# Performance work log

Hardware: AMD Instinct MI355X
Metric: run time of the kernel (lower is better)

The kernel has to match this reference:

```python
import jax, jax.numpy as jnp
import numpy as np

B, C, CI, T, H, W = 2, 1024, 512, 32, 14, 14
N = T * H * W


def setup_inputs() -> dict:
    key = jax.random.key(0)
    ks = jax.random.split(key, 6)
    s_in = 1.0 / np.sqrt(C)
    s_mid = 1.0 / np.sqrt(CI)
    return {
        "x": jax.random.normal(ks[0], (B, C, T, H, W), jnp.float32),
        "Wk": jax.random.normal(ks[1], (CI, C), jnp.float32) * s_in,
        "bk": jnp.zeros((CI,), jnp.float32),
        "Wq": jax.random.normal(ks[2], (CI, C), jnp.float32) * s_in,
        "bq": jnp.zeros((CI,), jnp.float32),
        "Wv": jax.random.normal(ks[3], (CI, C), jnp.float32) * s_in,
        "bv": jnp.zeros((CI,), jnp.float32),
        "Wo": jax.random.normal(ks[4], (C, CI), jnp.float32) * s_mid,
        "bo": jnp.zeros((C,), jnp.float32),
    }


def reference(x, Wk, bk, Wq, bq, Wv, bv, Wo, bo):
    # x: (B, C, T, H, W). Dropout layers are identity at inference.
    b, c, t, h, w = x.shape
    n = t * h * w
    xf = x.reshape(b, c, n)                          # (B, C, N)
    k = jnp.einsum("dc,bcn->bdn", Wk, xf) + bk[None, :, None]   # (B, CI, N)
    q = jnp.einsum("dc,bcn->bdn", Wq, xf) + bq[None, :, None]   # (B, CI, N)
    v = jnp.einsum("dc,bcn->bdn", Wv, xf) + bv[None, :, None]   # (B, CI, N)
    # alpha[b,i,j] = sum_d key[b,i,d] * query[b,d,j], scaled by 1/T
    alpha = jnp.einsum("bdi,bdj->bij", k, q) / float(t)          # (B, N, N)
    alpha = jax.nn.softmax(alpha, axis=-1)
    # y (B, CI, N) with y[b,c,i] = sum_j alpha[b,i,j] * v[b,c,j]
    y = jnp.einsum("bij,bcj->bci", alpha, v)
    out = jnp.einsum("dc,bcn->bdn", Wo, y) + bo[None, :, None]   # (B, C, N)
    return out.reshape(b, c, t, h, w) + x
```

## Files before the change

### kernel.cpp

```cpp
#include <hip/hip_runtime.h>

#define Bb 2
#define Cc 1024
#define CIi 512
#define Nn 6272
#define JH 3136
#define SCALE (1.0f / 32.0f)

typedef __bf16 bf16;
typedef __bf16 bf16x8 __attribute__((ext_vector_type(8)));
typedef __bf16 bf16x4 __attribute__((ext_vector_type(4)));
typedef float f32x4 __attribute__((ext_vector_type(4)));
typedef float f32x2 __attribute__((ext_vector_type(2)));
typedef unsigned int u32;
typedef unsigned int u32x4 __attribute__((ext_vector_type(4)));

__device__ __forceinline__ void g2l16(const void* g, void* l) {
  __builtin_amdgcn_global_load_lds(
      (const __attribute__((address_space(1))) u32*)g,
      (__attribute__((address_space(3))) u32*)(size_t)l, 16, 0, 0);
}

__global__ __launch_bounds__(256) void xpose_kernel(const float* __restrict__ x,
                                                    bf16* __restrict__ xT) {
  __shared__ float tile[32][33];
  int b = blockIdx.z;
  int n0 = blockIdx.x * 32, c0 = blockIdx.y * 32;
  int tn = threadIdx.x & 31, tr = threadIdx.x >> 5;
  const float* xp = x + ((size_t)b * Cc + c0) * Nn + n0;
  for (int i = 0; i < 4; i++) {
    int c = tr + i * 8;
    tile[c][tn] = xp[(size_t)c * Nn + tn];
  }
  __syncthreads();
  bf16* op = xT + ((size_t)b * Nn + n0) * Cc + c0;
  for (int i = 0; i < 4; i++) {
    int n = tr + i * 8;
    op[(size_t)n * Cc + tn] = (bf16)tile[tn][n];
  }
}

__global__ __launch_bounds__(256) void proj_kernel(
    const bf16* __restrict__ xT, const float* __restrict__ Wk,
    const float* __restrict__ Wq, const float* __restrict__ Wv,
    const float* __restrict__ bk, const float* __restrict__ bq,
    const float* __restrict__ bv, bf16* __restrict__ kT, bf16* __restrict__ qT,
    bf16* __restrict__ vv) {
  int z = blockIdx.z;
  int b = z / 3, proj = z % 3;
  const float* W = proj == 0 ? Wk : (proj == 1 ? Wq : Wv);
  const float* bias = proj == 0 ? bk : (proj == 1 ? bq : bv);
  int m0 = blockIdx.x * 128;
  int d0 = blockIdx.y * 128;
  __shared__ __align__(16) bf16 la[128 * 40];
  __shared__ __align__(16) bf16 lb[128 * 40];
  int tid = threadIdx.x;
  int wave = tid >> 6, lane = tid & 63, quad = lane >> 4, l16 = lane & 15;
  int wm = (wave >> 1) * 64, wn = (wave & 1) * 64;
  int row2 = tid >> 1, half = tid & 1;

  f32x4 acc[4][4] = {};
  const bf16* aSrc = xT + ((size_t)b * Nn + m0) * Cc;
  const float* bSrc = W + (size_t)(d0 + row2) * Cc;

  for (int k0 = 0; k0 < Cc; k0 += 32) {
    const u32x4* ga = (const u32x4*)(aSrc + (size_t)row2 * Cc + k0 + half * 16);
    u32x4 a0 = ga[0], a1 = ga[1];
    const f32x4* gb = (const f32x4*)(bSrc + k0 + half * 16);
    f32x4 w0 = gb[0], w1 = gb[1], w2 = gb[2], w3 = gb[3];
    *(u32x4*)&la[row2 * 40 + half * 16] = a0;
    *(u32x4*)&la[row2 * 40 + half * 16 + 8] = a1;
    bf16x8 p0 = {(bf16)w0[0], (bf16)w0[1], (bf16)w0[2], (bf16)w0[3],
                 (bf16)w1[0], (bf16)w1[1], (bf16)w1[2], (bf16)w1[3]};
    bf16x8 p1 = {(bf16)w2[0], (bf16)w2[1], (bf16)w2[2], (bf16)w2[3],
                 (bf16)w3[0], (bf16)w3[1], (bf16)w3[2], (bf16)w3[3]};
    *(bf16x8*)&lb[row2 * 40 + half * 16] = p0;
    *(bf16x8*)&lb[row2 * 40 + half * 16 + 8] = p1;
    __syncthreads();
    bf16x8 af[4], bfr[4];
    for (int t = 0; t < 4; t++)
      af[t] = *(const bf16x8*)&la[(wm + t * 16 + l16) * 40 + quad * 8];
    for (int t = 0; t < 4; t++)
      bfr[t] = *(const bf16x8*)&lb[(wn + t * 16 + l16) * 40 + quad * 8];
    for (int tm = 0; tm < 4; tm++)
      for (int tn = 0; tn < 4; tn++)
        acc[tm][tn] = __builtin_amdgcn_mfma_f32_16x16x32_bf16(
            af[tm], bfr[tn], acc[tm][tn], 0, 0, 0);
    __syncthreads();
  }
  for (int tn = 0; tn < 4; tn++) {
    int dcol = d0 + wn + tn * 16 + l16;
    float bval = bias[dcol];
    for (int tm = 0; tm < 4; tm++) {
      int nbase = m0 + wm + tm * 16 + quad * 4;
      for (int r = 0; r < 4; r++) {
        float val = acc[tm][tn][r] + bval;
        int nrow = nbase + r;
        if (proj == 0) {
          kT[((size_t)b * Nn + nrow) * CIi + dcol] = (bf16)val;
        } else if (proj == 1) {
          int ch = (dcol >> 3) ^ (nrow & 7);
          qT[((size_t)b * Nn + nrow) * CIi + ch * 8 + (dcol & 7)] = (bf16)val;
        } else {
          vv[((size_t)b * CIi + dcol) * Nn + nrow] = (bf16)val;
        }
      }
    }
  }
}

__global__ __launch_bounds__(512, 2) void attn_kernel(
    const bf16* __restrict__ kT, const bf16* __restrict__ qTs,
    const bf16* __restrict__ vv, bf16* __restrict__ yp,
    float* __restrict__ ml) {
  int l = blockIdx.x;
  int jh = l & 1, b = (l >> 1) & 1;
  int i0 = (l >> 2) * 128;
  int tid = threadIdx.x;
  int wave = tid >> 6, lane = tid & 63, quad = lane >> 4, l16 = lane & 15;
  int dw = wave * 64;

  __shared__ __align__(16) bf16 lq[2][32 * 512];
  __shared__ __align__(16) bf16 Psm[128 * 36];
  __shared__ float red[128];

  const bf16* qb = qTs + ((size_t)b * Nn + (size_t)jh * JH) * CIi;
  const bf16* vb = vv + (size_t)b * CIi * Nn + (size_t)jh * JH;

  bf16x8 kf[16];
  {
    const bf16* kp =
        kT + ((size_t)b * Nn + i0 + wave * 16 + l16) * CIi + quad * 8;
#pragma unroll
    for (int kk = 0; kk < 16; kk++) kf[kk] = *(const bf16x8*)(kp + kk * 32);
  }
  f32x4 oacc[8][4] = {};
  f32x4 l_acc = {};

  {
    const bf16* qrow = qb + (size_t)(wave * 4) * CIi + lane * 8;
#pragma unroll
    for (int r = 0; r < 4; r++)
      g2l16(qrow + (size_t)r * CIi, &lq[0][(wave * 4 + r) * 512]);
  }
  __syncthreads();

  int x0 = l16 & 7;
  for (int j0 = 0; j0 < JH; j0 += 32) {
    int t = (j0 >> 5) & 1;
    if (j0 + 32 < JH) {
      const bf16* qrow = qb + (size_t)(j0 + 32 + wave * 4) * CIi + lane * 8;
#pragma unroll
      for (int r = 0; r < 4; r++)
        g2l16(qrow + (size_t)r * CIi, &lq[t ^ 1][(wave * 4 + r) * 512]);
    }
    f32x4 s0 = {}, s1 = {};
    {
      const bf16* q0 = &lq[t][l16 * 512];
      const bf16* q1 = &lq[t][(16 + l16) * 512];
#pragma unroll
      for (int kk = 0; kk < 16; kk++) {
        int ch = (((kk * 4 + quad) ^ x0)) * 8;
        bf16x8 qf0 = *(const bf16x8*)(q0 + ch);
        bf16x8 qf1 = *(const bf16x8*)(q1 + ch);
        s0 = __builtin_amdgcn_mfma_f32_16x16x32_bf16(kf[kk], qf0, s0, 0, 0, 0);
        s1 = __builtin_amdgcn_mfma_f32_16x16x32_bf16(kf[kk], qf1, s1, 0, 0, 0);
      }
    }
    {
#pragma unroll
      for (int r = 0; r < 4; r++) {
        float p0 = __expf(fminf(fmaf(s0[r], SCALE, -2.0f), 20.0f));
        float p1 = __expf(fminf(fmaf(s1[r], SCALE, -2.0f), 20.0f));
        l_acc[r] += p0 + p1;
        int gi = wave * 16 + quad * 4 + r;
        Psm[gi * 36 + l16] = (bf16)p0;
        Psm[gi * 36 + 16 + l16] = (bf16)p1;
      }
    }
    __syncthreads();

    {
      u32x4 vf[4];
#pragma unroll
      for (int ds = 0; ds < 4; ds++)
        vf[ds] = *(const u32x4*)(vb + (size_t)(dw + ds * 16 + l16) * Nn + j0 +
                                 quad * 8);
#pragma unroll
      for (int is = 0; is < 8; is++) {
        bf16x8 pf = *(const bf16x8*)&Psm[(is * 16 + l16) * 36 + quad * 8];
#pragma unroll
        for (int ds = 0; ds < 4; ds++)
          oacc[is][ds] = __builtin_amdgcn_mfma_f32_16x16x32_bf16(
              pf, __builtin_bit_cast(bf16x8, vf[ds]), oacc[is][ds], 0, 0, 0);
      }
    }
    __syncthreads();
  }

#pragma unroll
  for (int o = 1; o < 16; o <<= 1)
#pragma unroll
    for (int r = 0; r < 4; r++) l_acc[r] += __shfl_xor(l_acc[r], o);
  if (l16 == 0) {
#pragma unroll
    for (int r = 0; r < 4; r++) {
      int gi = wave * 16 + quad * 4 + r;
      ml[(size_t)(jh * Bb + b) * Nn + i0 + gi] = l_acc[r];
      red[gi] = 1.0f / l_acc[r];
    }
  }
  __syncthreads();
  bf16* ypb = yp + ((size_t)jh * Bb + b) * Nn * CIi;
#pragma unroll
  for (int is = 0; is < 8; is++) {
    f32x4 inv = *(const f32x4*)&red[is * 16 + quad * 4];
#pragma unroll
    for (int ds = 0; ds < 4; ds++)
#pragma unroll
      for (int r = 0; r < 4; r++)
        ypb[(size_t)(i0 + is * 16 + quad * 4 + r) * CIi + dw + ds * 16 + l16] =
            (bf16)(oacc[is][ds][r] * inv[r]);
  }
}

__global__ __launch_bounds__(256) void merge_kernel(const bf16* __restrict__ yp,
                                                    const float* __restrict__ ml,
                                                    bf16* __restrict__ y) {
  int idx = blockIdx.x * 256 + threadIdx.x;
  int row = idx >> 6, c = idx & 63;
  float l0 = ml[row];
  float l1 = ml[(size_t)Bb * Nn + row];
  float inv = 1.0f / (l0 + l1);
  float w0 = l0 * inv, w1 = l1 * inv;
  bf16x8 v0 = *(const bf16x8*)&yp[(size_t)row * CIi + c * 8];
  bf16x8 v1 =
      *(const bf16x8*)&yp[(size_t)Bb * Nn * CIi + (size_t)row * CIi + c * 8];
  bf16x8 o;
#pragma unroll
  for (int k = 0; k < 8; k++)
    o[k] = (bf16)(w0 * (float)v0[k] + w1 * (float)v1[k]);
  *(bf16x8*)&y[(size_t)row * CIi + c * 8] = o;
}

__global__ __launch_bounds__(256) void out_kernel(
    const bf16* __restrict__ y, const float* __restrict__ Wo,
    const float* __restrict__ bo, const float* __restrict__ x,
    float* __restrict__ out) {
  int b = blockIdx.z;
  int d0 = blockIdx.x * 128;
  int m0 = blockIdx.y * 128;
  __shared__ __align__(16) bf16 la[128 * 40];
  __shared__ __align__(16) bf16 lb[128 * 40];
  int tid = threadIdx.x;
  int wave = tid >> 6, lane = tid & 63, quad = lane >> 4, l16 = lane & 15;
  int wm = (wave >> 1) * 64, wn = (wave & 1) * 64;
  int row2 = tid >> 1, half = tid & 1;
  f32x4 acc[4][4] = {};
  const float* aSrc = Wo + (size_t)(d0 + row2) * CIi;
  const bf16* bSrc = y + ((size_t)b * Nn + m0 + row2) * CIi;
  for (int k0 = 0; k0 < CIi; k0 += 32) {
    const f32x4* ga = (const f32x4*)(aSrc + k0 + half * 16);
    f32x4 w0 = ga[0], w1 = ga[1], w2 = ga[2], w3 = ga[3];
    const u32x4* gb = (const u32x4*)(bSrc + k0 + half * 16);
    u32x4 b0 = gb[0], b1 = gb[1];
    bf16x8 p0 = {(bf16)w0[0], (bf16)w0[1], (bf16)w0[2], (bf16)w0[3],
                 (bf16)w1[0], (bf16)w1[1], (bf16)w1[2], (bf16)w1[3]};
    bf16x8 p1 = {(bf16)w2[0], (bf16)w2[1], (bf16)w2[2], (bf16)w2[3],
                 (bf16)w3[0], (bf16)w3[1], (bf16)w3[2], (bf16)w3[3]};
    *(bf16x8*)&la[row2 * 40 + half * 16] = p0;
    *(bf16x8*)&la[row2 * 40 + half * 16 + 8] = p1;
    *(u32x4*)&lb[row2 * 40 + half * 16] = b0;
    *(u32x4*)&lb[row2 * 40 + half * 16 + 8] = b1;
    __syncthreads();
    bf16x8 af[4], bfr[4];
    for (int t = 0; t < 4; t++)
      af[t] = *(const bf16x8*)&la[(wm + t * 16 + l16) * 40 + quad * 8];
    for (int t = 0; t < 4; t++)
      bfr[t] = *(const bf16x8*)&lb[(wn + t * 16 + l16) * 40 + quad * 8];
    for (int tm = 0; tm < 4; tm++)
      for (int tn = 0; tn < 4; tn++)
        acc[tm][tn] = __builtin_amdgcn_mfma_f32_16x16x32_bf16(
            af[tm], bfr[tn], acc[tm][tn], 0, 0, 0);
    __syncthreads();
  }
  for (int tm = 0; tm < 4; tm++) {
    for (int r = 0; r < 4; r++) {
      int drow = d0 + wm + tm * 16 + quad * 4 + r;
      float bval = bo[drow];
      const float* xrow = x + ((size_t)b * Cc + drow) * Nn;
      float* orow = out + ((size_t)b * Cc + drow) * Nn;
      for (int tn = 0; tn < 4; tn++) {
        int ncol = m0 + wn + tn * 16 + l16;
        orow[ncol] = acc[tm][tn][r] + bval + xrow[ncol];
      }
    }
  }
}

extern "C" void kernel_launch(void* const* d_in, const int* in_sizes, int n_in,
                              void* d_out, int out_size, void* d_ws,
                              size_t ws_size, hipStream_t stream) {
  (void)in_sizes;
  (void)n_in;
  (void)out_size;
  (void)ws_size;
  const float* x = (const float*)d_in[0];
  const float* Wk = (const float*)d_in[1];
  const float* bk = (const float*)d_in[2];
  const float* Wq = (const float*)d_in[3];
  const float* bq = (const float*)d_in[4];
  const float* Wv = (const float*)d_in[5];
  const float* bv = (const float*)d_in[6];
  const float* Wo = (const float*)d_in[7];
  const float* bo = (const float*)d_in[8];
  float* out = (float*)d_out;

  bf16* xT = (bf16*)d_ws;
  bf16* yp = (bf16*)d_ws;
  bf16* y = (bf16*)d_ws + (size_t)Bb * Nn * Cc;
  bf16* kT = (bf16*)d_out;
  bf16* qT = kT + (size_t)Bb * Nn * CIi;
  bf16* vv = qT + (size_t)Bb * Nn * CIi;
  float* ml = (float*)((char*)d_out + (size_t)40 * 1024 * 1024);

  xpose_kernel<<<dim3(Nn / 32, Cc / 32, Bb), 256, 0, stream>>>(x, xT);
  proj_kernel<<<dim3(Nn / 128, CIi / 128, 3 * Bb), 256, 0, stream>>>(
      xT, Wk, Wq, Wv, bk, bq, bv, kT, qT, vv);
  attn_kernel<<<dim3((Nn / 128) * 2 * Bb), 512, 0, stream>>>(kT, qT, vv, yp,
                                                             ml);
  merge_kernel<<<dim3(Bb * Nn * 64 / 256), 256, 0, stream>>>(yp, ml, y);
  out_kernel<<<dim3(Cc / 128, Nn / 128, Bb), 256, 0, stream>>>(y, Wo, bo, x,
                                                               out);
}
```

Baseline: 579.3 us.

## Split attention key range into four partitions instead of two

The attention kernel now splits the key/value range into four quarters instead of two, doubling the grid so more workgroups are available to fill the CUs. The merge kernel combines four partial outputs, weighted by their softmax denominators. The occupancy hint rises from 2 to 4 blocks, which squeezes the per-thread register budget while each thread still holds large accumulator and K-fragment arrays, so spilling is a real risk. LDS use per block limits actual residency anyway, and the larger partial buffer means the merged output now aliases part of the partial-result workspace.

```diff
diff --git a/kernel.cpp b/kernel.cpp
--- a/kernel.cpp
+++ b/kernel.cpp
@@ -4,7 +4,7 @@
 #define Cc 1024
 #define CIi 512
 #define Nn 6272
-#define JH 3136
+#define JQ 1568
 #define SCALE (1.0f / 32.0f)
 
 typedef __bf16 bf16;
@@ -109,13 +109,13 @@
   }
 }
 
-__global__ __launch_bounds__(512, 2) void attn_kernel(
+__global__ __launch_bounds__(512, 4) void attn_kernel(
     const bf16* __restrict__ kT, const bf16* __restrict__ qTs,
     const bf16* __restrict__ vv, bf16* __restrict__ yp,
     float* __restrict__ ml) {
   int l = blockIdx.x;
-  int jh = l & 1, b = (l >> 1) & 1;
-  int i0 = (l >> 2) * 128;
+  int jq = l & 3, b = (l >> 2) & 1;
+  int i0 = (l >> 3) * 128;
   int tid = threadIdx.x;
   int wave = tid >> 6, lane = tid & 63, quad = lane >> 4, l16 = lane & 15;
   int dw = wave * 64;
@@ -124,8 +124,8 @@
   __shared__ __align__(16) bf16 Psm[128 * 36];
   __shared__ float red[128];
 
-  const bf16* qb = qTs + ((size_t)b * Nn + (size_t)jh * JH) * CIi;
-  const bf16* vb = vv + (size_t)b * CIi * Nn + (size_t)jh * JH;
+  const bf16* qb = qTs + ((size_t)b * Nn + (size_t)jq * JQ) * CIi;
+  const bf16* vb = vv + (size_t)b * CIi * Nn + (size_t)jq * JQ;
 
   bf16x8 kf[16];
   {
@@ -146,9 +146,9 @@
   __syncthreads();
 
   int x0 = l16 & 7;
-  for (int j0 = 0; j0 < JH; j0 += 32) {
+  for (int j0 = 0; j0 < JQ; j0 += 32) {
     int t = (j0 >> 5) & 1;
-    if (j0 + 32 < JH) {
+    if (j0 + 32 < JQ) {
       const bf16* qrow = qb + (size_t)(j0 + 32 + wave * 4) * CIi + lane * 8;
 #pragma unroll
       for (int r = 0; r < 4; r++)
@@ -206,12 +206,12 @@
 #pragma unroll
     for (int r = 0; r < 4; r++) {
       int gi = wave * 16 + quad * 4 + r;
-      ml[(size_t)(jh * Bb + b) * Nn + i0 + gi] = l_acc[r];
+      ml[(size_t)(jq * Bb + b) * Nn + i0 + gi] = l_acc[r];
       red[gi] = 1.0f / l_acc[r];
     }
   }
   __syncthreads();
-  bf16* ypb = yp + ((size_t)jh * Bb + b) * Nn * CIi;
+  bf16* ypb = yp + ((size_t)jq * Bb + b) * Nn * CIi;
 #pragma unroll
   for (int is = 0; is < 8; is++) {
     f32x4 inv = *(const f32x4*)&red[is * 16 + quad * 4];
@@ -229,17 +229,27 @@
                                                     bf16* __restrict__ y) {
   int idx = blockIdx.x * 256 + threadIdx.x;
   int row = idx >> 6, c = idx & 63;
-  float l0 = ml[row];
-  float l1 = ml[(size_t)Bb * Nn + row];
-  float inv = 1.0f / (l0 + l1);
-  float w0 = l0 * inv, w1 = l1 * inv;
-  bf16x8 v0 = *(const bf16x8*)&yp[(size_t)row * CIi + c * 8];
-  bf16x8 v1 =
-      *(const bf16x8*)&yp[(size_t)Bb * Nn * CIi + (size_t)row * CIi + c * 8];
+  float ls[4];
+  float tot = 0.0f;
+#pragma unroll
+  for (int s = 0; s < 4; s++) {
+    ls[s] = ml[(size_t)s * Bb * Nn + row];
+    tot += ls[s];
+  }
+  float inv = 1.0f / tot;
+  float acc[8] = {};
+#pragma unroll
+  for (int s = 0; s < 4; s++) {
+    float w = ls[s] * inv;
+    bf16x8 v =
+        *(const bf16x8*)&yp[(size_t)s * Bb * Nn * CIi + (size_t)row * CIi +
+                            c * 8];
+#pragma unroll
+    for (int k = 0; k < 8; k++) acc[k] += w * (float)v[k];
+  }
   bf16x8 o;
 #pragma unroll
-  for (int k = 0; k < 8; k++)
-    o[k] = (bf16)(w0 * (float)v0[k] + w1 * (float)v1[k]);
+  for (int k = 0; k < 8; k++) o[k] = (bf16)acc[k];
   *(bf16x8*)&y[(size_t)row * CIi + c * 8] = o;
 }
 
@@ -327,7 +337,7 @@
   xpose_kernel<<<dim3(Nn / 32, Cc / 32, Bb), 256, 0, stream>>>(x, xT);
   proj_kernel<<<dim3(Nn / 128, CIi / 128, 3 * Bb), 256, 0, stream>>>(
       xT, Wk, Wq, Wv, bk, bq, bv, kT, qT, vv);
-  attn_kernel<<<dim3((Nn / 128) * 2 * Bb), 512, 0, stream>>>(kT, qT, vv, yp,
+  attn_kernel<<<dim3((Nn / 128) * 4 * Bb), 512, 0, stream>>>(kT, qT, vv, yp,
                                                              ml);
   merge_kernel<<<dim3(Bb * Nn * 64 / 256), 256, 0, stream>>>(yp, ml, y);
   out_kernel<<<dim3(Cc / 128, Nn / 128, Bb), 256, 0, stream>>>(y, Wo, bo, x,
```

New measurement: 1.506 ms. 160% more time.
